# Optimization experiments

Measured on AMD Instinct MI355X. Metric: run time of the kernel, lower is better.

The kernel has to match this reference:

```python
import jax, jax.numpy as jnp
import numpy as np

B, V, T, C, HIN, WIN = 1, 6, 3, 256, 32, 32
NH = 8
LN_EPS = 1e-5


def setup_inputs() -> dict:
    key = jax.random.key(0)
    ks = jax.random.split(key, 14)
    s = 0.02
    lim = 1.0 / np.sqrt(C)
    def lin_w(k):
        return jax.random.uniform(k, (C, C), jnp.float32, -lim, lim)
    return {
        "history_feats": jax.random.normal(ks[0], (B, V, T, C, HIN, WIN), jnp.float32),
        "query_embed": jax.random.normal(ks[1], (1, C, 1, 1), jnp.float32) * s,
        "camera_pos_embed": jax.random.normal(ks[2], (V, C), jnp.float32) * s,
        "temporal_pos_embed": jax.random.normal(ks[3], (T, C), jnp.float32) * s,
        "spatial_pos_embed": jax.random.normal(ks[4], (1, C, 1, 1), jnp.float32) * s,
        "q_w": lin_w(ks[5]), "q_b": jnp.zeros((C,), jnp.float32),
        "k_w": lin_w(ks[6]), "k_b": jnp.zeros((C,), jnp.float32),
        "v_w": lin_w(ks[7]), "v_b": jnp.zeros((C,), jnp.float32),
        "o_w": lin_w(ks[8]), "o_b": jnp.zeros((C,), jnp.float32),
        "ln_g": jnp.ones((C,), jnp.float32),
        "ln_b": jnp.zeros((C,), jnp.float32),
        "query_cam_idx": 0,
        "H": 32,
        "W": 32,
    }


def reference(history_feats, query_embed, camera_pos_embed, temporal_pos_embed,
              spatial_pos_embed, q_w, q_b, k_w, k_b, v_w, v_b, o_w, o_b,
              ln_g, ln_b, query_cam_idx, H, W):
    B_, V_, T_, C_, Hin, Win = history_feats.shape
    dh = C_ // NH
    # --- build query: [B, H*W, C] ---
    q = query_embed + camera_pos_embed[query_cam_idx][None, :, None, None] + spatial_pos_embed
    q = jnp.broadcast_to(q, (B_, C_, H, W)).reshape(B_, C_, H * W).transpose(0, 2, 1)
    kv = (history_feats
          + temporal_pos_embed[None, None, :, :, None, None]
          + camera_pos_embed[None, :, None, :, None, None])
    kv = kv.transpose(0, 1, 2, 4, 5, 3).reshape(B_, V_ * T_ * Hin * Win, C_)
    # --- projections (torch Linear: x @ W.T + b) ---
    qp = q @ q_w.T + q_b
    kp = kv @ k_w.T + k_b
    vp = kv @ v_w.T + v_b
    # --- split heads: [B, NH, L, dh] ---
    qh = qp.reshape(B_, H * W, NH, dh).transpose(0, 2, 1, 3)
    kh = kp.reshape(B_, -1, NH, dh).transpose(0, 2, 1, 3)
    vh = vp.reshape(B_, -1, NH, dh).transpose(0, 2, 1, 3)
    scale = float(dh) ** -0.5
    attn = jax.nn.softmax(jnp.einsum('bhqd,bhkd->bhqk', qh, kh) * scale, axis=-1)
    out = jnp.einsum('bhqk,bhkd->bhqd', attn, vh)
    out = out.transpose(0, 2, 1, 3).reshape(B_, H * W, C_)
    out = out @ o_w.T + o_b
    # --- LayerNorm over channel dim ---
    mu = out.mean(-1, keepdims=True)
    var = ((out - mu) ** 2).mean(-1, keepdims=True)
    out = (out - mu) * jax.lax.rsqrt(var + LN_EPS) * ln_g + ln_b
    return out.transpose(0, 2, 1).reshape(B_, C_, H, W)
```

## Files before the change

kernel.cpp:

```cpp
#include <hip/hip_runtime.h>

typedef const float* fcp;

#define C_    256
#define NH_   8
#define DH_   32
#define VT_   18
#define HWK   1024
#define L_    (VT_*HWK)
#define SCALE_ 0.17677669529663687f

#define EMB_OFF  0
#define WF_OFF   4608
#define BB_OFF   6656
#define PS_OFF   6720
#define CTX_OFF  9088
#define Y_OFF    11136
#define Z_OFF    11392
#define PEX_OFF  11648

__device__ __forceinline__ float blockReduceSum256(float v){
  __shared__ float red[4];
  #pragma unroll
  for (int off = 32; off; off >>= 1) v += __shfl_xor(v, off, 64);
  const int lane = threadIdx.x & 63, w = threadIdx.x >> 6;
  __syncthreads();
  if (lane == 0) red[w] = v;
  __syncthreads();
  return red[0] + red[1] + red[2] + red[3];
}

__global__ void k_fold(fcp qe, fcp cam, fcp tpe, fcp spe, const int* __restrict__ cidx,
                       fcp qw, fcp qb, fcp kw, fcp kb, float* __restrict__ ws){
  __shared__ float qvS[C_];
  __shared__ float qpS[DH_];
  const int b = blockIdx.x, t = threadIdx.x, lane = t & 63, wv = t >> 6;
  const int ci = cidx[0];
  qvS[t] = qe[t] + cam[ci*C_ + t] + spe[t];
  {
    const int v = b/3, tt = b - v*3;
    ws[EMB_OFF + b*C_ + t] = tpe[tt*C_ + t] + cam[v*C_ + t];
  }
  if (b == 17){
    #pragma unroll
    for (int i = 0; i < 8; i++) ws[CTX_OFF + i*C_ + t] = 0.f;
  }
  __syncthreads();
  if (b < 8){
    #pragma unroll
    for (int i = 0; i < 8; i++){
      const int r = b*DH_ + wv*8 + i;
      fcp qr = qw + (size_t)r*C_;
      float v = qr[lane]*qvS[lane] + qr[64+lane]*qvS[64+lane]
              + qr[128+lane]*qvS[128+lane] + qr[192+lane]*qvS[192+lane];
      #pragma unroll
      for (int off = 32; off; off >>= 1) v += __shfl_xor(v, off, 64);
      if (lane == 0) qpS[wv*8 + i] = v + qb[r];
    }
    __syncthreads();
    float acc = 0.f;
    #pragma unroll 8
    for (int d = 0; d < DH_; d++)
      acc += qpS[d] * kw[(size_t)(b*DH_ + d)*C_ + t];
    ws[WF_OFF + b*C_ + t] = SCALE_ * acc;
    if (t == 0){
      float bb = 0.f;
      for (int d = 0; d < DH_; d++) bb += qpS[d] * kb[b*DH_ + d];
      ws[BB_OFF + b] = SCALE_ * bb;
    }
  }
}

__global__ void k_scores(fcp feats, float* __restrict__ ws){
  __shared__ __align__(16) float wf[C_*8];
  __shared__ float redS[32];
  __shared__ float basef[8];
  __shared__ __align__(16) float pred[8*512];
  const int bid = blockIdx.x, vt = bid >> 4, sc = bid & 15, t = threadIdx.x;

  for (int idx = t; idx < 2048; idx += 512){
    const int h = idx >> 8, c = idx & 255;
    wf[c*8 + h] = ws[WF_OFF + idx];
  }
  __syncthreads();
  if (t < 256){
    const float e = ws[EMB_OFF + vt*C_ + t];
    const float4 wa = *(const float4*)&wf[t*8];
    const float4 wb = *(const float4*)&wf[t*8 + 4];
    float pb[8] = {e*wa.x, e*wa.y, e*wa.z, e*wa.w, e*wb.x, e*wb.y, e*wb.z, e*wb.w};
    #pragma unroll
    for (int h = 0; h < 8; h++){
      float v = pb[h];
      #pragma unroll
      for (int off = 32; off; off >>= 1) v += __shfl_xor(v, off, 64);
      if ((t & 63) == 0) redS[(t >> 6)*8 + h] = v;
    }
  }
  __syncthreads();
  if (t < 8) basef[t] = redS[t] + redS[8+t] + redS[16+t] + redS[24+t] + ws[BB_OFF + t];
  __syncthreads();
  const int s = t & 63, cg = t >> 6;
  const int gb = vt*HWK + sc*64;
  fcp fp = feats + ((size_t)vt*C_ + cg*32)*HWK + sc*64 + s;
  float acc[8] = {0,0,0,0,0,0,0,0};
  #pragma unroll 8
  for (int i = 0; i < 32; i++){
    const float fv = fp[(size_t)i*HWK];
    const float4 wa = *(const float4*)&wf[(cg*32+i)*8];
    const float4 wb = *(const float4*)&wf[(cg*32+i)*8 + 4];
    acc[0] += fv*wa.x; acc[1] += fv*wa.y; acc[2] += fv*wa.z; acc[3] += fv*wa.w;
    acc[4] += fv*wb.x; acc[5] += fv*wb.y; acc[6] += fv*wb.z; acc[7] += fv*wb.w;
  }
  #pragma unroll
  for (int h = 0; h < 8; h++) pred[cg*512 + h*64 + s] = acc[h];
  __syncthreads();
  const int h1 = t >> 6, tok = t & 63;
  float sum = basef[h1];
  #pragma unroll
  for (int cg2 = 0; cg2 < 8; cg2++) sum += pred[cg2*512 + t];
  const float e = __expf(sum);
  ws[PEX_OFF + (size_t)(gb + tok)*8 + h1] = e;
  float v = e;
  #pragma unroll
  for (int off = 32; off; off >>= 1) v += __shfl_xor(v, off, 64);
  if (tok == 0) ws[PS_OFF + bid*8 + h1] = v;
}

__global__ void k_ctx(fcp feats, float* __restrict__ ws){
  const int bid = blockIdx.x;
  const int vt = bid / 64, r = bid - vt*64, cc = r & 15, ssi = r >> 4;
  const int t = threadIdx.x, wv = t >> 6, lane = t & 63;
  const int c0 = cc*16 + wv*4;
  fcp fb = feats + (size_t)vt*C_*HWK + ssi*256;
  const float* pexb = ws + PEX_OFF + ((size_t)vt*HWK + ssi*256)*8;
  float acc[4][8];
  #pragma unroll
  for (int j = 0; j < 4; j++)
    #pragma unroll
    for (int h = 0; h < 8; h++) acc[j][h] = 0.f;

  #pragma unroll
  for (int step = 0; step < 4; step++){
    const int s = step*64 + lane;
    const float4 pa = *(const float4*)(pexb + (size_t)s*8);
    const float4 pb = *(const float4*)(pexb + (size_t)s*8 + 4);
    #pragma unroll
    for (int j = 0; j < 4; j++){
      const float fv = fb[(size_t)(c0 + j)*HWK + s];
      acc[j][0] += fv*pa.x; acc[j][1] += fv*pa.y; acc[j][2] += fv*pa.z; acc[j][3] += fv*pa.w;
      acc[j][4] += fv*pb.x; acc[j][5] += fv*pb.y; acc[j][6] += fv*pb.z; acc[j][7] += fv*pb.w;
    }
  }
  #pragma unroll
  for (int j = 0; j < 4; j++)
    #pragma unroll
    for (int h = 0; h < 8; h++){
      float v = acc[j][h];
      #pragma unroll
      for (int off = 32; off; off >>= 1) v += __shfl_xor(v, off, 64);
      if (lane == j*8 + h) atomicAdd(ws + CTX_OFF + h*C_ + c0 + j, v);
    }
}

__global__ void k_vproj(fcp vw, fcp vb, float* __restrict__ ws){
  __shared__ float psS[288*8];
  const int r = blockIdx.x, t = threadIdx.x, h = r >> 5;
  for (int i = t; i < 288*8; i += 256) psS[i] = ws[PS_OFF + i];
  __syncthreads();
  float denom = 0.f, embP = 0.f;
  for (int vt = 0; vt < VT_; vt++){
    float P = 0.f;
    #pragma unroll
    for (int sc2 = 0; sc2 < 16; sc2++) P += psS[(vt*16 + sc2)*8 + h];
    denom += P;
    embP  += ws[EMB_OFF + vt*C_ + t] * P;
  }
  const float ctxn = (ws[CTX_OFF + h*C_ + t] + embP) / denom;
  float v = vw[(size_t)r*C_ + t] * ctxn;
  v = blockReduceSum256(v);
  if (t == 0) ws[Y_OFF + r] = v + vb[r];
}

__global__ void k_oproj(fcp ow, fcp ob, float* __restrict__ ws){
  const int r = blockIdx.x, t = threadIdx.x;
  float v = ow[(size_t)r*C_ + t] * ws[Y_OFF + t];
  v = blockReduceSum256(v);
  if (t == 0) ws[Z_OFF + r] = v + ob[r];
}

__global__ void k_out(fcp lng, fcp lnb, const float* __restrict__ ws,
                      float* __restrict__ out, int hw){
  const int c = blockIdx.x, t = threadIdx.x;
  const float z = ws[Z_OFF + t];
  const float s  = blockReduceSum256(z);
  const float s2 = blockReduceSum256(z*z);
  const float mu = s * (1.f/C_);
  const float var = s2 * (1.f/C_) - mu*mu;
  const float rs = rsqrtf(var + 1e-5f);
  const float fin = (ws[Z_OFF + c] - mu) * rs * lng[c] + lnb[c];
  float4 pk = make_float4(fin, fin, fin, fin);
  ((float4*)(out + (size_t)c*hw))[t] = pk;
}

extern "C" void kernel_launch(void* const* d_in, const int* in_sizes, int n_in,
                              void* d_out, int out_size, void* d_ws, size_t ws_size,
                              hipStream_t stream) {
  fcp feats = (fcp)d_in[0];
  fcp qe    = (fcp)d_in[1];
  fcp cam   = (fcp)d_in[2];
  fcp tpe   = (fcp)d_in[3];
  fcp spe   = (fcp)d_in[4];
  fcp qw    = (fcp)d_in[5];
  fcp qb    = (fcp)d_in[6];
  fcp kw    = (fcp)d_in[7];
  fcp kb    = (fcp)d_in[8];
  fcp vw    = (fcp)d_in[9];
  fcp vb    = (fcp)d_in[10];
  fcp ow    = (fcp)d_in[11];
  fcp ob    = (fcp)d_in[12];
  fcp lng   = (fcp)d_in[13];
  fcp lnb   = (fcp)d_in[14];
  const int* cidx = (const int*)d_in[15];
  float* ws = (float*)d_ws;
  float* out = (float*)d_out;
  const int hw = out_size / C_;

  k_fold  <<<18,   256, 0, stream>>>(qe, cam, tpe, spe, cidx, qw, qb, kw, kb, ws);
  k_scores<<<288,  512, 0, stream>>>(feats, ws);
  k_ctx   <<<1152, 256, 0, stream>>>(feats, ws);
  k_vproj <<<256,  256, 0, stream>>>(vw, vb, ws);
  k_oproj <<<256,  256, 0, stream>>>(ow, ob, ws);
  k_out   <<<256,  256, 0, stream>>>(lng, lnb, ws, out, hw);
}
```

Measured before the change: 159.3 us.

## Fuse score and context kernels, staging features in fp16 shared memory

Merges the score/exp kernel with the context-accumulation kernel. Each block stages its 256x64 feature tile in shared memory as fp16 and computes per-block partial context sums, which are written to workspace instead of being accumulated with atomics. The vproj kernel then reduces the 288 partials. This avoids reading the large feature tensor from global memory a second time and removes the exp-value round trip and the atomics. In exchange it adds a large shared-memory footprint that may lower occupancy, fp16 rounding in the context sums, and a serial 288-way reduction inside vproj.

```diff
diff --git a/kernel.cpp b/kernel.cpp
--- a/kernel.cpp
+++ b/kernel.cpp
@@ -1,4 +1,5 @@
 #include <hip/hip_runtime.h>
+#include <hip/hip_fp16.h>
 
 typedef const float* fcp;
 
@@ -14,10 +15,9 @@
 #define WF_OFF   4608
 #define BB_OFF   6656
 #define PS_OFF   6720
-#define CTX_OFF  9088
-#define Y_OFF    11136
-#define Z_OFF    11392
-#define PEX_OFF  11648
+#define Y_OFF    9024
+#define Z_OFF    9280
+#define CTXP_OFF 9536
 
 __device__ __forceinline__ float blockReduceSum256(float v){
   __shared__ float red[4];
@@ -40,10 +40,6 @@
   {
     const int v = b/3, tt = b - v*3;
     ws[EMB_OFF + b*C_ + t] = tpe[tt*C_ + t] + cam[v*C_ + t];
-  }
-  if (b == 17){
-    #pragma unroll
-    for (int i = 0; i < 8; i++) ws[CTX_OFF + i*C_ + t] = 0.f;
   }
   __syncthreads();
   if (b < 8){
@@ -71,11 +67,13 @@
   }
 }
 
-__global__ void k_scores(fcp feats, float* __restrict__ ws){
+__global__ void k_attn(fcp feats, float* __restrict__ ws){
   __shared__ __align__(16) float wf[C_*8];
   __shared__ float redS[32];
   __shared__ float basef[8];
   __shared__ __align__(16) float pred[8*512];
+  __shared__ float pexS[64*8];
+  __shared__ __half fS[8*32*66];
   const int bid = blockIdx.x, vt = bid >> 4, sc = bid & 15, t = threadIdx.x;
 
   for (int idx = t; idx < 2048; idx += 512){
@@ -100,12 +98,12 @@
   if (t < 8) basef[t] = redS[t] + redS[8+t] + redS[16+t] + redS[24+t] + ws[BB_OFF + t];
   __syncthreads();
   const int s = t & 63, cg = t >> 6;
-  const int gb = vt*HWK + sc*64;
   fcp fp = feats + ((size_t)vt*C_ + cg*32)*HWK + sc*64 + s;
   float acc[8] = {0,0,0,0,0,0,0,0};
   #pragma unroll 8
   for (int i = 0; i < 32; i++){
     const float fv = fp[(size_t)i*HWK];
+    fS[(cg*32 + i)*66 + s] = __float2half(fv);
     const float4 wa = *(const float4*)&wf[(cg*32+i)*8];
     const float4 wb = *(const float4*)&wf[(cg*32+i)*8 + 4];
     acc[0] += fv*wa.x; acc[1] += fv*wa.y; acc[2] += fv*wa.z; acc[3] += fv*wa.w;
@@ -114,52 +112,32 @@
   #pragma unroll
   for (int h = 0; h < 8; h++) pred[cg*512 + h*64 + s] = acc[h];
   __syncthreads();
-  const int h1 = t >> 6, tok = t & 63;
-  float sum = basef[h1];
+  {
+    const int h1 = t >> 6, tok = t & 63;
+    float sum = basef[h1];
+    #pragma unroll
+    for (int cg2 = 0; cg2 < 8; cg2++) sum += pred[cg2*512 + t];
+    const float e = __expf(sum);
+    pexS[tok*8 + h1] = e;
+    float v = e;
+    #pragma unroll
+    for (int off = 32; off; off >>= 1) v += __shfl_xor(v, off, 64);
+    if (tok == 0) ws[PS_OFF + bid*8 + h1] = v;
+  }
+  __syncthreads();
+  const int lane = t & 63, hB = lane & 7, isub = lane >> 3;
+  float aB[4] = {0.f, 0.f, 0.f, 0.f};
+  #pragma unroll 8
+  for (int s2 = 0; s2 < 64; s2++){
+    const float pe = pexS[s2*8 + hB];
+    #pragma unroll
+    for (int p = 0; p < 4; p++)
+      aB[p] += pe * __half2float(fS[(cg*32 + p*8 + isub)*66 + s2]);
+  }
+  float* outp = ws + CTXP_OFF + (size_t)bid*2048;
   #pragma unroll
-  for (int cg2 = 0; cg2 < 8; cg2++) sum += pred[cg2*512 + t];
-  const float e = __expf(sum);
-  ws[PEX_OFF + (size_t)(gb + tok)*8 + h1] = e;
-  float v = e;
-  #pragma unroll
-  for (int off = 32; off; off >>= 1) v += __shfl_xor(v, off, 64);
-  if (tok == 0) ws[PS_OFF + bid*8 + h1] = v;
-}
-
-__global__ void k_ctx(fcp feats, float* __restrict__ ws){
-  const int bid = blockIdx.x;
-  const int vt = bid / 64, r = bid - vt*64, cc = r & 15, ssi = r >> 4;
-  const int t = threadIdx.x, wv = t >> 6, lane = t & 63;
-  const int c0 = cc*16 + wv*4;
-  fcp fb = feats + (size_t)vt*C_*HWK + ssi*256;
-  const float* pexb = ws + PEX_OFF + ((size_t)vt*HWK + ssi*256)*8;
-  float acc[4][8];
-  #pragma unroll
-  for (int j = 0; j < 4; j++)
-    #pragma unroll
-    for (int h = 0; h < 8; h++) acc[j][h] = 0.f;
-
-  #pragma unroll
-  for (int step = 0; step < 4; step++){
-    const int s = step*64 + lane;
-    const float4 pa = *(const float4*)(pexb + (size_t)s*8);
-    const float4 pb = *(const float4*)(pexb + (size_t)s*8 + 4);
-    #pragma unroll
-    for (int j = 0; j < 4; j++){
-      const float fv = fb[(size_t)(c0 + j)*HWK + s];
-      acc[j][0] += fv*pa.x; acc[j][1] += fv*pa.y; acc[j][2] += fv*pa.z; acc[j][3] += fv*pa.w;
-      acc[j][4] += fv*pb.x; acc[j][5] += fv*pb.y; acc[j][6] += fv*pb.z; acc[j][7] += fv*pb.w;
-    }
-  }
-  #pragma unroll
-  for (int j = 0; j < 4; j++)
-    #pragma unroll
-    for (int h = 0; h < 8; h++){
-      float v = acc[j][h];
-      #pragma unroll
-      for (int off = 32; off; off >>= 1) v += __shfl_xor(v, off, 64);
-      if (lane == j*8 + h) atomicAdd(ws + CTX_OFF + h*C_ + c0 + j, v);
-    }
+  for (int p = 0; p < 4; p++)
+    outp[hB*256 + cg*32 + p*8 + isub] = aB[p];
 }
 
 __global__ void k_vproj(fcp vw, fcp vb, float* __restrict__ ws){
@@ -167,6 +145,10 @@
   const int r = blockIdx.x, t = threadIdx.x, h = r >> 5;
   for (int i = t; i < 288*8; i += 256) psS[i] = ws[PS_OFF + i];
   __syncthreads();
+  float ctx = 0.f;
+  const float* pp = ws + CTXP_OFF + h*256 + t;
+  #pragma unroll 8
+  for (int b = 0; b < 288; b++) ctx += pp[(size_t)b*2048];
   float denom = 0.f, embP = 0.f;
   for (int vt = 0; vt < VT_; vt++){
     float P = 0.f;
@@ -175,7 +157,7 @@
     denom += P;
     embP  += ws[EMB_OFF + vt*C_ + t] * P;
   }
-  const float ctxn = (ws[CTX_OFF + h*C_ + t] + embP) / denom;
+  const float ctxn = (ctx + embP) / denom;
   float v = vw[(size_t)r*C_ + t] * ctxn;
   v = blockReduceSum256(v);
   if (t == 0) ws[Y_OFF + r] = v + vb[r];
@@ -225,10 +207,9 @@
   float* out = (float*)d_out;
   const int hw = out_size / C_;
 
-  k_fold  <<<18,   256, 0, stream>>>(qe, cam, tpe, spe, cidx, qw, qb, kw, kb, ws);
-  k_scores<<<288,  512, 0, stream>>>(feats, ws);
-  k_ctx   <<<1152, 256, 0, stream>>>(feats, ws);
-  k_vproj <<<256,  256, 0, stream>>>(vw, vb, ws);
-  k_oproj <<<256,  256, 0, stream>>>(ow, ob, ws);
-  k_out   <<<256,  256, 0, stream>>>(lng, lnb, ws, out, hw);
-}
+  k_fold  <<<18,  256, 0, stream>>>(qe, cam, tpe, spe, cidx, qw, qb, kw, kb, ws);
+  k_attn  <<<288, 512, 0, stream>>>(feats, ws);
+  k_vproj <<<256, 256, 0, stream>>>(vw, vb, ws);
+  k_oproj <<<256, 256, 0, stream>>>(ow, ob, ws);
+  k_out   <<<256, 256, 0, stream>>>(lng, lnb, ws, out, hw);
+}
```

Result: faster. 148.2 us (-6.9%).
